# Optimization experiments

Measured on AMD Instinct MI355X. Metric: run time of the kernel, lower is better.

## Reference

```python
import jax, jax.numpy as jnp
import numpy as np

N_NODES = 100000
N_EDGES = 1600000
D = 64
BN_EPS = 1e-5


def setup_inputs() -> dict:
    key = jax.random.key(0)
    ks = jax.random.split(key, 10)
    s = 1.0 / np.sqrt(D)
    return {
        "features": jax.random.normal(ks[0], (N_NODES, D), dtype=jnp.float32),
        "src": jax.random.randint(ks[1], (N_EDGES,), 0, N_NODES, dtype=jnp.int32),
        "dst": jax.random.randint(ks[2], (N_EDGES,), 0, N_NODES, dtype=jnp.int32),
        "eps": jnp.zeros((), dtype=jnp.float32),
        "W1": jax.random.uniform(ks[3], (D, D), jnp.float32, -s, s),
        "b1": jax.random.uniform(ks[4], (D,), jnp.float32, -s, s),
        "W2": jax.random.uniform(ks[5], (D, D), jnp.float32, -s, s),
        "b2": jax.random.uniform(ks[6], (D,), jnp.float32, -s, s),
        "gamma": jnp.ones((D,), dtype=jnp.float32),
        "beta": jnp.zeros((D,), dtype=jnp.float32),
    }


def reference(features, src, dst, eps, W1, b1, W2, b2, gamma, beta):
    h_in = features
    # message passing: gather src node features, scatter-sum to dst (fn.copy_u + fn.sum)
    neigh = jax.ops.segment_sum(features[src], dst, num_segments=N_NODES)  # [N, D]
    # eps-weighted self term
    h = (1.0 + eps) * features + neigh
    # apply_func MLP: Linear -> ReLU -> Linear
    h = jnp.maximum(h @ W1 + b1, 0.0) @ W2 + b2
    # BatchNorm1d over nodes (training-mode batch statistics)
    mean = jnp.mean(h, axis=0)
    var = jnp.var(h, axis=0)
    h = (h - mean) * jax.lax.rsqrt(var + BN_EPS) * gamma + beta
    # activation
    h = jnp.maximum(h, 0.0)
    # residual (indim == outdim)
    h = h_in + h
    # dropout p=0 -> identity
    return h
```

## Files before the change

### kernel.cpp

```cpp
#include <hip/hip_runtime.h>
#include <hip/hip_fp16.h>

#define N_NODES 100000
#define N_EDGES 1600000
#define D 64
#define BN_EPS 1e-5f
#define NBKT 256
#define NPB 391
#define BKT_CAP 7680
#define SORT_T 1024
#define NSHARD 64

typedef _Float16 half8 __attribute__((ext_vector_type(8)));
typedef float f32x4 __attribute__((ext_vector_type(4)));

__global__ __launch_bounds__(256) void bucket_k(
    const int* __restrict__ src, const int* __restrict__ dst,
    int* __restrict__ bkt_cnt, int2* __restrict__ bktbuf)
{
    __shared__ int h[NBKT], base[NBKT], cur[NBKT];
    const int t = threadIdx.x;
    if (t < NBKT) { h[t] = 0; cur[t] = 0; }
    __syncthreads();
    const int e0 = blockIdx.x * 4096;
    int s[16], d[16], b[16];
    #pragma unroll
    for (int i = 0; i < 16; ++i) {
        int e = e0 + i * 256 + t;
        if (e < N_EDGES) {
            s[i] = src[e];
            d[i] = dst[e];
            b[i] = d[i] / NPB;
            atomicAdd(&h[b[i]], 1);
        } else {
            b[i] = -1;
        }
    }
    __syncthreads();
    if (t < NBKT) base[t] = atomicAdd(&bkt_cnt[t], h[t]);
    __syncthreads();
    #pragma unroll
    for (int i = 0; i < 16; ++i) {
        if (b[i] >= 0) {
            int p = atomicAdd(&cur[b[i]], 1);
            bktbuf[(size_t)b[i] * BKT_CAP + base[b[i]] + p] = make_int2(s[i], d[i]);
        }
    }
}

__global__ __launch_bounds__(SORT_T) void sort_k(
    const int2* __restrict__ bktbuf, const int* __restrict__ bkt_cnt,
    int* __restrict__ rowptr, int* __restrict__ col)
{
    __shared__ int h[NPB];
    __shared__ int cur[NPB];
    __shared__ int part[SORT_T];
    __shared__ int bsc[NBKT];

    const int b = blockIdx.x;
    const int t = threadIdx.x;
    const int nb0 = b * NPB;
    const int nodes_in = min(NPB, N_NODES - nb0);
    const int cnt = bkt_cnt[b];
    const int2* buf = bktbuf + (size_t)b * BKT_CAP;

    if (t < NBKT) bsc[t] = bkt_cnt[t];
    __syncthreads();
    for (int off = 1; off < NBKT; off <<= 1) {
        int x = 0;
        if (t < NBKT) {
            x = bsc[t];
            if (t >= off) x += bsc[t - off];
        }
        __syncthreads();
        if (t < NBKT) bsc[t] = x;
        __syncthreads();
    }
    const int gbase = bsc[b] - cnt;

    if (t < NPB) h[t] = 0;
    __syncthreads();

    for (int i = t; i < cnt; i += SORT_T)
        atomicAdd(&h[buf[i].y - nb0], 1);
    __syncthreads();

    int a = (t < NPB) ? h[t] : 0;
    part[t] = a;
    __syncthreads();
    for (int off = 1; off < SORT_T; off <<= 1) {
        int x = part[t];
        int u = (t >= off) ? part[t - off] : 0;
        __syncthreads();
        part[t] = x + u;
        __syncthreads();
    }
    int excl = part[t] - a;
    if (t < NPB) {
        cur[t] = excl;
        if (t < nodes_in) rowptr[nb0 + t] = gbase + excl;
    }
    if (b == NBKT - 1 && t == 0) rowptr[N_NODES] = N_EDGES;
    __syncthreads();

    for (int i = t; i < cnt; i += SORT_T) {
        int2 r = buf[i];
        int slot = atomicAdd(&cur[r.y - nb0], 1);
        col[gbase + slot] = r.x;
    }
}

__global__ __launch_bounds__(256) void conv_k(
    const float* __restrict__ feat, __half* __restrict__ feat16)
{
    size_t i = ((size_t)blockIdx.x * 256 + threadIdx.x) * 8;
    if (i < (size_t)N_NODES * D) {
        float4 v0 = *(const float4*)(feat + i);
        float4 v1 = *(const float4*)(feat + i + 4);
        __half2 o[4];
        o[0] = __floats2half2_rn(v0.x, v0.y);
        o[1] = __floats2half2_rn(v0.z, v0.w);
        o[2] = __floats2half2_rn(v1.x, v1.y);
        o[3] = __floats2half2_rn(v1.z, v1.w);
        *(float4*)(feat16 + i) = *(float4*)o;
    }
}

__global__ __launch_bounds__(256) void wprep_k(
    const float* __restrict__ W1, const float* __restrict__ W2,
    _Float16* __restrict__ w1t, _Float16* __restrict__ w2t)
{
    const int t = threadIdx.x;
    const int n = t >> 2;
    const int k0 = (t & 3) * 16;
    _Float16 o1[16], o2[16];
    #pragma unroll
    for (int j = 0; j < 16; ++j) {
        o1[j] = (_Float16)W1[(k0 + j) * 64 + n];
        o2[j] = (_Float16)W2[(k0 + j) * 64 + n];
    }
    #pragma unroll
    for (int j = 0; j < 16; j += 8) {
        *(half8*)(w1t + n * 64 + k0 + j) = *(half8*)&o1[j];
        *(half8*)(w2t + n * 64 + k0 + j) = *(half8*)&o2[j];
    }
}

__global__ __launch_bounds__(256) void gather16_k(
    const __half* __restrict__ feat16, const int* __restrict__ rowptr,
    const int* __restrict__ col, const float* __restrict__ epsp,
    __half* __restrict__ x16)
{
    int node = blockIdx.x * 4 + (threadIdx.x >> 6);
    int lane = threadIdx.x & 63;
    if (node >= N_NODES) return;
    int g = lane >> 3;
    int c = (lane & 7) << 3;
    int lo = rowptr[node];
    int hi = rowptr[node + 1];
    float a[8] = {0.f, 0.f, 0.f, 0.f, 0.f, 0.f, 0.f, 0.f};
    int e = lo + g;
    for (; e + 8 < hi; e += 16) {
        int s0 = col[e];
        int s1 = col[e + 8];
        float4 r0 = *(const float4*)(feat16 + (size_t)s0 * D + c);
        float4 r1 = *(const float4*)(feat16 + (size_t)s1 * D + c);
        const __half2* h0 = (const __half2*)&r0;
        const __half2* h1 = (const __half2*)&r1;
        #pragma unroll
        for (int i = 0; i < 4; ++i) {
            float2 f0 = __half22float2(h0[i]);
            float2 f1 = __half22float2(h1[i]);
            a[2 * i]     += f0.x + f1.x;
            a[2 * i + 1] += f0.y + f1.y;
        }
    }
    if (e < hi) {
        float4 r0 = *(const float4*)(feat16 + (size_t)col[e] * D + c);
        const __half2* h0 = (const __half2*)&r0;
        #pragma unroll
        for (int i = 0; i < 4; ++i) {
            float2 f0 = __half22float2(h0[i]);
            a[2 * i]     += f0.x;
            a[2 * i + 1] += f0.y;
        }
    }
    #pragma unroll
    for (int off = 8; off <= 32; off <<= 1)
        #pragma unroll
        for (int i = 0; i < 8; ++i)
            a[i] += __shfl_xor(a[i], off, 64);
    if (g == 0) {
        float4 rs = *(const float4*)(feat16 + (size_t)node * D + c);
        const __half2* hs = (const __half2*)&rs;
        const float epsv = 1.0f + epsp[0];
        __half2 o[4];
        #pragma unroll
        for (int i = 0; i < 4; ++i) {
            float2 fs = __half22float2(hs[i]);
            o[i] = __floats2half2_rn(fmaf(epsv, fs.x, a[2 * i]),
                                     fmaf(epsv, fs.y, a[2 * i + 1]));
        }
        *(float4*)(x16 + (size_t)node * D + c) = *(float4*)o;
    }
}

__global__ __launch_bounds__(256) void gather32_k(
    const float* __restrict__ feat, const int* __restrict__ rowptr,
    const int* __restrict__ col, const float* __restrict__ epsp,
    float* __restrict__ x)
{
    int node = blockIdx.x * 4 + (threadIdx.x >> 6);
    int lane = threadIdx.x & 63;
    if (node >= N_NODES) return;
    int g = lane >> 4;
    int c = (lane & 15) << 2;
    int lo = rowptr[node];
    int hi = rowptr[node + 1];
    float ax = 0.f, ay = 0.f, az = 0.f, aw = 0.f;
    int e = lo + g;
    for (; e + 4 < hi; e += 8) {
        int s0 = col[e];
        int s1 = col[e + 4];
        float4 v0 = *(const float4*)(feat + (size_t)s0 * D + c);
        float4 v1 = *(const float4*)(feat + (size_t)s1 * D + c);
        ax += v0.x; ay += v0.y; az += v0.z; aw += v0.w;
        ax += v1.x; ay += v1.y; az += v1.z; aw += v1.w;
    }
    if (e < hi) {
        float4 v = *(const float4*)(feat + (size_t)col[e] * D + c);
        ax += v.x; ay += v.y; az += v.z; aw += v.w;
    }
    #pragma unroll
    for (int off = 16; off <= 32; off <<= 1) {
        ax += __shfl_xor(ax, off, 64);
        ay += __shfl_xor(ay, off, 64);
        az += __shfl_xor(az, off, 64);
        aw += __shfl_xor(aw, off, 64);
    }
    if (g == 0) {
        float4 f = *(const float4*)(feat + (size_t)node * D + c);
        const float epsv = 1.0f + epsp[0];
        float4 r;
        r.x = fmaf(epsv, f.x, ax);
        r.y = fmaf(epsv, f.y, ay);
        r.z = fmaf(epsv, f.z, az);
        r.w = fmaf(epsv, f.w, aw);
        *(float4*)(x + (size_t)node * D + c) = r;
    }
}

__global__ __launch_bounds__(256) void mfma_mlp2_k(
    const __half* __restrict__ x16,
    const _Float16* __restrict__ w1t, const _Float16* __restrict__ w2t,
    const float* __restrict__ b1, const float* __restrict__ b2,
    __half* __restrict__ h216, float* __restrict__ stats)
{
    __shared__ __align__(16) _Float16 xts[64 * 72];

    const int t    = threadIdx.x;
    const int w    = t >> 6;
    const int lane = t & 63;
    const int m    = lane & 15;
    const int q    = lane >> 4;
    const int rbase = w * 16;
    const int nb   = blockIdx.x * 64;

    const _Float16* xg = (const _Float16*)x16 + (size_t)(nb + rbase + m) * 64 + q * 8;
    half8 a0 = *(const half8*)(xg);
    half8 a1 = *(const half8*)(xg + 32);

    f32x4 acc[4];
    #pragma unroll
    for (int jt = 0; jt < 4; ++jt) {
        const float bias = b1[jt * 16 + m];
        acc[jt] = (f32x4){bias, bias, bias, bias};
        const _Float16* bw = w1t + (jt * 16 + m) * 64 + q * 8;
        half8 bf0 = *(const half8*)(bw);
        half8 bf1 = *(const half8*)(bw + 32);
        acc[jt] = __builtin_amdgcn_mfma_f32_16x16x32_f16(a0, bf0, acc[jt], 0, 0, 0);
        acc[jt] = __builtin_amdgcn_mfma_f32_16x16x32_f16(a1, bf1, acc[jt], 0, 0, 0);
    }

    #pragma unroll
    for (int jt = 0; jt < 4; ++jt)
        #pragma unroll
        for (int r = 0; r < 4; ++r)
            xts[(rbase + q * 4 + r) * 72 + jt * 16 + m] =
                (_Float16)fmaxf(acc[jt][r], 0.0f);
    asm volatile("s_waitcnt lgkmcnt(0)" ::: "memory");

    const _Float16* xw = &xts[(rbase + m) * 72 + q * 8];
    half8 c0 = *(const half8*)(xw);
    half8 c1 = *(const half8*)(xw + 32);

    f32x4 acc2[4];
    #pragma unroll
    for (int jt = 0; jt < 4; ++jt) {
        const float bias = b2[jt * 16 + m];
        acc2[jt] = (f32x4){bias, bias, bias, bias};
        const _Float16* bw = w2t + (jt * 16 + m) * 64 + q * 8;
        half8 bf0 = *(const half8*)(bw);
        half8 bf1 = *(const half8*)(bw + 32);
        acc2[jt] = __builtin_amdgcn_mfma_f32_16x16x32_f16(c0, bf0, acc2[jt], 0, 0, 0);
        acc2[jt] = __builtin_amdgcn_mfma_f32_16x16x32_f16(c1, bf1, acc2[jt], 0, 0, 0);
    }
    asm volatile("s_waitcnt lgkmcnt(0)" ::: "memory");

    float psums[4], psqs[4];
    #pragma unroll
    for (int jt = 0; jt < 4; ++jt) {
        float ps = 0.f, pq = 0.f;
        #pragma unroll
        for (int r = 0; r < 4; ++r) {
            const int row = rbase + q * 4 + r;
            const float v = acc2[jt][r];
            const float vv = (nb + row < N_NODES) ? v : 0.f;
            ps += vv;
            pq += vv * vv;
            xts[row * 72 + jt * 16 + m] = (_Float16)v;
        }
        ps += __shfl_xor(ps, 16, 64); ps += __shfl_xor(ps, 32, 64);
        pq += __shfl_xor(pq, 16, 64); pq += __shfl_xor(pq, 32, 64);
        psums[jt] = ps; psqs[jt] = pq;
    }
    if (lane < 16) {
        float* sp = stats + (size_t)(blockIdx.x & (NSHARD - 1)) * 128;
        #pragma unroll
        for (int jt = 0; jt < 4; ++jt) {
            unsafeAtomicAdd(sp + jt * 16 + lane,      psums[jt]);
            unsafeAtomicAdd(sp + 64 + jt * 16 + lane, psqs[jt]);
        }
    }
    asm volatile("s_waitcnt lgkmcnt(0)" ::: "memory");

    {
        const int rr = lane >> 2;
        const int cc = (lane & 3) * 16;
        const int gn = nb + rbase + rr;
        if (gn < N_NODES) {
            float4 r0 = *(const float4*)&xts[(rbase + rr) * 72 + cc];
            float4 r1 = *(const float4*)&xts[(rbase + rr) * 72 + cc + 8];
            *(float4*)(h216 + (size_t)gn * 64 + cc)     = r0;
            *(float4*)(h216 + (size_t)gn * 64 + cc + 8) = r1;
        }
    }
}

__global__ __launch_bounds__(256) void mlp32_k(
    const float* __restrict__ x,
    const float* __restrict__ W1, const float* __restrict__ b1,
    const float* __restrict__ W2, const float* __restrict__ b2,
    float* __restrict__ h2out, float* __restrict__ stats)
{
    __shared__ float W1s[64 * 68];
    __shared__ float W2s[64 * 68];
    __shared__ float xs[64 * 65];
    __shared__ float b1s[64], b2s[64];

    const int t  = threadIdx.x;
    const int nb = blockIdx.x * 64;

    #pragma unroll
    for (int i = 0; i < 4; ++i) {
        int l  = t + i * 256;
        int k  = l >> 4;
        int j4 = (l & 15) << 2;
        *(float4*)(&W1s[k * 68 + j4]) = *(const float4*)(W1 + k * 64 + j4);
        *(float4*)(&W2s[k * 68 + j4]) = *(const float4*)(W2 + k * 64 + j4);
    }
    if (t < 64)       b1s[t]      = b1[t];
    else if (t < 128) b2s[t - 64] = b2[t - 64];

    #pragma unroll
    for (int i = 0; i < 2; ++i) {
        int n  = (t >> 3) + i * 32;
        int k8 = (t & 7) << 3;
        int gn = nb + n;
        float4 a = make_float4(0.f, 0.f, 0.f, 0.f), b = a;
        if (gn < N_NODES) {
            a = *(const float4*)(x + (size_t)gn * D + k8);
            b = *(const float4*)(x + (size_t)gn * D + k8 + 4);
        }
        *(float4*)&xs[n * 65 + k8]     = a;
        *(float4*)&xs[n * 65 + k8 + 4] = b;
    }
    __syncthreads();

    const int n0 = (t & 15) << 2;
    const int j0 = (t >> 4) << 2;
    const float* xr0 = &xs[(n0 + 0) * 65];
    const float* xr1 = &xs[(n0 + 1) * 65];
    const float* xr2 = &xs[(n0 + 2) * 65];
    const float* xr3 = &xs[(n0 + 3) * 65];

    float acc[4][4];
    #pragma unroll
    for (int a = 0; a < 4; ++a)
        #pragma unroll
        for (int b = 0; b < 4; ++b)
            acc[a][b] = b1s[j0 + b];

    #pragma unroll 8
    for (int k = 0; k < 64; ++k) {
        const float4 w = *(const float4*)(&W1s[k * 68 + j0]);
        const float x0 = xr0[k], x1 = xr1[k], x2 = xr2[k], x3 = xr3[k];
        acc[0][0] = fmaf(x0, w.x, acc[0][0]); acc[0][1] = fmaf(x0, w.y, acc[0][1]);
        acc[0][2] = fmaf(x0, w.z, acc[0][2]); acc[0][3] = fmaf(x0, w.w, acc[0][3]);
        acc[1][0] = fmaf(x1, w.x, acc[1][0]); acc[1][1] = fmaf(x1, w.y, acc[1][1]);
        acc[1][2] = fmaf(x1, w.z, acc[1][2]); acc[1][3] = fmaf(x1, w.w, acc[1][3]);
        acc[2][0] = fmaf(x2, w.x, acc[2][0]); acc[2][1] = fmaf(x2, w.y, acc[2][1]);
        acc[2][2] = fmaf(x2, w.z, acc[2][2]); acc[2][3] = fmaf(x2, w.w, acc[2][3]);
        acc[3][0] = fmaf(x3, w.x, acc[3][0]); acc[3][1] = fmaf(x3, w.y, acc[3][1]);
        acc[3][2] = fmaf(x3, w.z, acc[3][2]); acc[3][3] = fmaf(x3, w.w, acc[3][3]);
    }

    __syncthreads();
    #pragma unroll
    for (int a = 0; a < 4; ++a)
        #pragma unroll
        for (int b = 0; b < 4; ++b)
            xs[(n0 + a) * 65 + j0 + b] = fmaxf(acc[a][b], 0.0f);
    __syncthreads();

    float acc2[4][4];
    #pragma unroll
    for (int a = 0; a < 4; ++a)
        #pragma unroll
        for (int b = 0; b < 4; ++b)
            acc2[a][b] = b2s[j0 + b];

    #pragma unroll 8
    for (int k = 0; k < 64; ++k) {
        const float4 w = *(const float4*)(&W2s[k * 68 + j0]);
        const float x0 = xr0[k], x1 = xr1[k], x2 = xr2[k], x3 = xr3[k];
        acc2[0][0] = fmaf(x0, w.x, acc2[0][0]); acc2[0][1] = fmaf(x0, w.y, acc2[0][1]);
        acc2[0][2] = fmaf(x0, w.z, acc2[0][2]); acc2[0][3] = fmaf(x0, w.w, acc2[0][3]);
        acc2[1][0] = fmaf(x1, w.x, acc2[1][0]); acc2[1][1] = fmaf(x1, w.y, acc2[1][1]);
        acc2[1][2] = fmaf(x1, w.z, acc2[1][2]); acc2[1][3] = fmaf(x1, w.w, acc2[1][3]);
        acc2[2][0] = fmaf(x2, w.x, acc2[2][0]); acc2[2][1] = fmaf(x2, w.y, acc2[2][1]);
        acc2[2][2] = fmaf(x2, w.z, acc2[2][2]); acc2[2][3] = fmaf(x2, w.w, acc2[2][3]);
        acc2[3][0] = fmaf(x3, w.x, acc2[3][0]); acc2[3][1] = fmaf(x3, w.y, acc2[3][1]);
        acc2[3][2] = fmaf(x3, w.z, acc2[3][2]); acc2[3][3] = fmaf(x3, w.w, acc2[3][3]);
    }

    float psum[4] = {0.f, 0.f, 0.f, 0.f};
    float psq[4]  = {0.f, 0.f, 0.f, 0.f};
    #pragma unroll
    for (int a = 0; a < 4; ++a) {
        int gn = nb + n0 + a;
        if (gn < N_NODES) {
            float4 hh;
            hh.x = acc2[a][0]; hh.y = acc2[a][1]; hh.z = acc2[a][2]; hh.w = acc2[a][3];
            *(float4*)(h2out + (size_t)gn * 64 + j0) = hh;
            psum[0] += hh.x; psq[0] += hh.x * hh.x;
            psum[1] += hh.y; psq[1] += hh.y * hh.y;
            psum[2] += hh.z; psq[2] += hh.z * hh.z;
            psum[3] += hh.w; psq[3] += hh.w * hh.w;
        }
    }
    #pragma unroll
    for (int off = 8; off >= 1; off >>= 1)
        #pragma unroll
        for (int b = 0; b < 4; ++b) {
            psum[b] += __shfl_down(psum[b], off, 16);
            psq[b]  += __shfl_down(psq[b],  off, 16);
        }
    if ((t & 15) == 0) {
        float* sp = stats + (size_t)(blockIdx.x & (NSHARD - 1)) * 128;
        #pragma unroll
        for (int b = 0; b < 4; ++b) {
            unsafeAtomicAdd(sp + j0 + b,      psum[b]);
            unsafeAtomicAdd(sp + 64 + j0 + b, psq[b]);
        }
    }
}

__global__ void bnstats_k(const float* __restrict__ stats,
                          const float* __restrict__ gamma,
                          const float* __restrict__ beta,
                          float* __restrict__ sf)
{
    int j = threadIdx.x;
    float s = 0.f, q = 0.f;
    for (int c = 0; c < NSHARD; ++c) {
        s += stats[c * 128 + j];
        q += stats[c * 128 + 64 + j];
    }
    const float invN = 1.0f / (float)N_NODES;
    float mean  = s * invN;
    float var   = q * invN - mean * mean;
    float scale = gamma[j] * rsqrtf(var + BN_EPS);
    sf[j]      = scale;
    sf[64 + j] = beta[j] - mean * scale;
}

__global__ __launch_bounds__(256) void finish16_k(
    const float* __restrict__ feat, const __half* __restrict__ h216,
    const float* __restrict__ sf, float* __restrict__ out)
{
    __shared__ float scs[64], shs[64];
    if (threadIdx.x < 64) {
        scs[threadIdx.x] = sf[threadIdx.x];
        shs[threadIdx.x] = sf[64 + threadIdx.x];
    }
    __syncthreads();
    size_t i = (size_t)blockIdx.x * 256 + threadIdx.x;
    if (i < (size_t)N_NODES * D / 4) {
        int j = (int)((i * 4) & 63);
        const __half2* hp = (const __half2*)(h216 + i * 4);
        float2 h0 = __half22float2(hp[0]);
        float2 h1 = __half22float2(hp[1]);
        float4 f = *(const float4*)(feat + i * 4);
        float4 o;
        o.x = fmaxf(fmaf(h0.x, scs[j + 0], shs[j + 0]), 0.f) + f.x;
        o.y = fmaxf(fmaf(h0.y, scs[j + 1], shs[j + 1]), 0.f) + f.y;
        o.z = fmaxf(fmaf(h1.x, scs[j + 2], shs[j + 2]), 0.f) + f.z;
        o.w = fmaxf(fmaf(h1.y, scs[j + 3], shs[j + 3]), 0.f) + f.w;
        *(float4*)(out + i * 4) = o;
    }
}

__global__ __launch_bounds__(256) void finish_k(
    const float* __restrict__ feat, const float* __restrict__ sf,
    float* __restrict__ out)
{
    __shared__ float scs[64], shs[64];
    if (threadIdx.x < 64) {
        scs[threadIdx.x] = sf[threadIdx.x];
        shs[threadIdx.x] = sf[64 + threadIdx.x];
    }
    __syncthreads();
    size_t i = (size_t)blockIdx.x * 256 + threadIdx.x;
    if (i < (size_t)N_NODES * D / 4) {
        int j = (int)((i * 4) & 63);
        float4 h = *(float4*)(out + i * 4);
        float4 f = *(const float4*)(feat + i * 4);
        h.x = fmaxf(fmaf(h.x, scs[j + 0], shs[j + 0]), 0.f) + f.x;
        h.y = fmaxf(fmaf(h.y, scs[j + 1], shs[j + 1]), 0.f) + f.y;
        h.z = fmaxf(fmaf(h.z, scs[j + 2], shs[j + 2]), 0.f) + f.z;
        h.w = fmaxf(fmaf(h.w, scs[j + 3], shs[j + 3]), 0.f) + f.w;
        *(float4*)(out + i * 4) = h;
    }
}

extern "C" void kernel_launch(void* const* d_in, const int* in_sizes, int n_in,
                              void* d_out, int out_size, void* d_ws, size_t ws_size,
                              hipStream_t stream)
{
    const float* feat  = (const float*)d_in[0];
    const int*   src   = (const int*)d_in[1];
    const int*   dst   = (const int*)d_in[2];
    const float* eps   = (const float*)d_in[3];
    const float* W1    = (const float*)d_in[4];
    const float* b1    = (const float*)d_in[5];
    const float* W2    = (const float*)d_in[6];
    const float* b2    = (const float*)d_in[7];
    const float* gamma = (const float*)d_in[8];
    const float* beta  = (const float*)d_in[9];
    float* out = (float*)d_out;

    const size_t BKTSZ = (size_t)NBKT * BKT_CAP * sizeof(int2);
    const size_t F16SZ = (size_t)N_NODES * D * sizeof(__half);
    const size_t X32SZ = (size_t)N_NODES * D * sizeof(float);
    const size_t COLSZ = (size_t)N_EDGES * sizeof(int);
    const size_t RPSZ  = (size_t)(N_NODES + 1) * sizeof(int);
    const size_t STATSZ = (size_t)NSHARD * 128 * sizeof(float);
    const size_t TAIL  = STATSZ + NBKT * 4 + 128 * 4 + 2 * 4096 * sizeof(_Float16) + 256;
    const size_t need16 = BKTSZ + F16SZ + COLSZ + RPSZ + TAIL;

    if (ws_size >= need16) {
        char* p = (char*)d_ws;
        __half* x16    = (__half*)p;
        int2*   bktbuf = (int2*)p;
        __half* feat16 = (__half*)(p + BKTSZ);
        __half* h216   = (__half*)(p + BKTSZ);
        int*    col    = (int*)(p + BKTSZ + F16SZ);
        int*    rowptr = col + N_EDGES;
        float*  stats  = (float*)(rowptr + N_NODES + 1);
        int*    bkt_cnt = (int*)(stats + NSHARD * 128);
        float*  sf     = (float*)(bkt_cnt + NBKT);
        _Float16* w1t  = (_Float16*)(sf + 128);
        _Float16* w2t  = w1t + 4096;

        hipMemsetAsync(stats, 0, STATSZ + NBKT * 4, stream);
        conv_k<<<3125, 256, 0, stream>>>(feat, feat16);
        wprep_k<<<1, 256, 0, stream>>>(W1, W2, w1t, w2t);
        bucket_k<<<(N_EDGES + 4095) / 4096, 256, 0, stream>>>(src, dst, bkt_cnt, bktbuf);
        sort_k<<<NBKT, SORT_T, 0, stream>>>(bktbuf, bkt_cnt, rowptr, col);
        gather16_k<<<(N_NODES + 3) / 4, 256, 0, stream>>>(feat16, rowptr, col, eps, x16);
        mfma_mlp2_k<<<(N_NODES + 63) / 64, 256, 0, stream>>>(x16, w1t, w2t, b1, b2, h216, stats);
        bnstats_k<<<1, 64, 0, stream>>>(stats, gamma, beta, sf);
        finish16_k<<<(N_NODES * D / 4 + 255) / 256, 256, 0, stream>>>(feat, h216, sf, out);
    } else {
        char* p = (char*)d_ws;
        float* x32    = (float*)p;
        int2*  bktbuf = (int2*)p;
        int*   col    = (int*)(p + X32SZ);
        int*   rowptr = col + N_EDGES;
        float* stats  = (float*)(rowptr + N_NODES + 1);
        int*   bkt_cnt = (int*)(stats + NSHARD * 128);
        float* sf     = (float*)(bkt_cnt + NBKT);

        hipMemsetAsync(stats, 0, STATSZ + NBKT * 4, stream);
        bucket_k<<<(N_EDGES + 4095) / 4096, 256, 0, stream>>>(src, dst, bkt_cnt, bktbuf);
        sort_k<<<NBKT, SORT_T, 0, stream>>>(bktbuf, bkt_cnt, rowptr, col);
        gather32_k<<<(N_NODES + 3) / 4, 256, 0, stream>>>(feat, rowptr, col, eps, x32);
        mlp32_k<<<(N_NODES + 63) / 64, 256, 0, stream>>>(x32, W1, b1, W2, b2, out, stats);
        bnstats_k<<<1, 64, 0, stream>>>(stats, gamma, beta, sf);
        finish_k<<<(N_NODES * D / 4 + 255) / 256, 256, 0, stream>>>(feat, sf, out);
    }
}
```

Measured before the change: 221.9 us.

## Replace CSR sort+gather with bucketed LDS atomic scatter and fused prep kernel

Drops the full counting sort into CSR. Edges are now packed into 782 fine-grained buckets of 128 destination nodes each, storing src<<7|local_dst in a single int, inside a fused prep kernel that also does the fp16 feature conversion and the weight transpose. A new scatter kernel accumulates neighbour features into a swizzled LDS tile with shared-memory float atomics, then adds the eps self term and writes x16. This removes the sort pass, the rowptr/col arrays and two launches. In exchange it relies on LDS atomics and a fixed bucket capacity of 2560 that silently truncates if a bucket overflows.

```diff
diff --git a/kernel.cpp b/kernel.cpp
--- a/kernel.cpp
+++ b/kernel.cpp
@@ -5,22 +5,316 @@
 #define N_EDGES 1600000
 #define D 64
 #define BN_EPS 1e-5f
-#define NBKT 256
-#define NPB 391
-#define BKT_CAP 7680
+#define NSHARD 64
+
+#define NBKT 782
+#define NPB 128
+#define BKT_CAP 2560
+#define NBBLK 391
+#define ACC_LD 68
+
+#define ONBKT 256
+#define ONPB 391
+#define OCAP 7680
 #define SORT_T 1024
-#define NSHARD 64
 
 typedef _Float16 half8 __attribute__((ext_vector_type(8)));
 typedef float f32x4 __attribute__((ext_vector_type(4)));
 
-__global__ __launch_bounds__(256) void bucket_k(
+__global__ __launch_bounds__(256) void prep_k(
+    const int* __restrict__ src, const int* __restrict__ dst,
+    int* __restrict__ bkt_cnt, int* __restrict__ bktbuf,
+    const float* __restrict__ feat, __half* __restrict__ feat16,
+    const float* __restrict__ W1, const float* __restrict__ W2,
+    _Float16* __restrict__ w1t, _Float16* __restrict__ w2t)
+{
+    __shared__ int h[NBKT], base[NBKT], cur[NBKT];
+    const int blk = blockIdx.x;
+    const int t = threadIdx.x;
+
+    if (blk < NBBLK) {
+        for (int i = t; i < NBKT; i += 256) { h[i] = 0; cur[i] = 0; }
+        __syncthreads();
+        const int e0 = blk * 4096;
+        int pk[16], b[16];
+        #pragma unroll
+        for (int i = 0; i < 16; ++i) {
+            int e = e0 + i * 256 + t;
+            if (e < N_EDGES) {
+                int d = dst[e];
+                b[i] = d >> 7;
+                pk[i] = (src[e] << 7) | (d & 127);
+                atomicAdd(&h[b[i]], 1);
+            } else {
+                b[i] = -1;
+            }
+        }
+        __syncthreads();
+        for (int i = t; i < NBKT; i += 256)
+            if (h[i]) base[i] = atomicAdd(&bkt_cnt[i], h[i]);
+        __syncthreads();
+        #pragma unroll
+        for (int i = 0; i < 16; ++i) {
+            if (b[i] >= 0) {
+                int p = atomicAdd(&cur[b[i]], 1);
+                bktbuf[(size_t)b[i] * BKT_CAP + base[b[i]] + p] = pk[i];
+            }
+        }
+    } else if (blk < NBBLK + 3125) {
+        size_t i = ((size_t)(blk - NBBLK) * 256 + t) * 8;
+        if (i < (size_t)N_NODES * D) {
+            float4 v0 = *(const float4*)(feat + i);
+            float4 v1 = *(const float4*)(feat + i + 4);
+            __half2 o[4];
+            o[0] = __floats2half2_rn(v0.x, v0.y);
+            o[1] = __floats2half2_rn(v0.z, v0.w);
+            o[2] = __floats2half2_rn(v1.x, v1.y);
+            o[3] = __floats2half2_rn(v1.z, v1.w);
+            *(float4*)(feat16 + i) = *(float4*)o;
+        }
+    } else {
+        const int n = t >> 2;
+        const int k0 = (t & 3) * 16;
+        _Float16 o1[16], o2[16];
+        #pragma unroll
+        for (int j = 0; j < 16; ++j) {
+            o1[j] = (_Float16)W1[(k0 + j) * 64 + n];
+            o2[j] = (_Float16)W2[(k0 + j) * 64 + n];
+        }
+        #pragma unroll
+        for (int j = 0; j < 16; j += 8) {
+            *(half8*)(w1t + n * 64 + k0 + j) = *(half8*)&o1[j];
+            *(half8*)(w2t + n * 64 + k0 + j) = *(half8*)&o2[j];
+        }
+    }
+}
+
+__global__ __launch_bounds__(512, 8) void scatter16_k(
+    const int* __restrict__ bktbuf, const int* __restrict__ bkt_cnt,
+    const __half* __restrict__ feat16, const float* __restrict__ epsp,
+    __half* __restrict__ x16)
+{
+    __shared__ float acc[NPB * ACC_LD];
+    const int b = blockIdx.x;
+    const int t = threadIdx.x;
+    const int nb0 = b * NPB;
+    const int cnt = min(bkt_cnt[b], BKT_CAP);
+    const int* __restrict__ buf = bktbuf + (size_t)b * BKT_CAP;
+
+    for (int i = t; i < NPB * ACC_LD; i += 512) acc[i] = 0.f;
+    __syncthreads();
+
+    const int g0 = t >> 3;
+    const int k  = t & 7;
+    const int c  = k << 3;
+
+    int e = g0;
+    int pk = (e < cnt) ? buf[e] : 0;
+    while (e < cnt) {
+        const int en = e + 64;
+        const int pkn = (en < cnt) ? buf[en] : 0;
+        const int srow = pk >> 7;
+        const int drow = pk & 127;
+        float4 r = *(const float4*)(feat16 + (size_t)srow * 64 + c);
+        const __half2* hh = (const __half2*)&r;
+        float f[8];
+        #pragma unroll
+        for (int i = 0; i < 4; ++i) {
+            float2 fv = __half22float2(hh[i]);
+            f[2 * i]     = fv.x;
+            f[2 * i + 1] = fv.y;
+        }
+        float* rowp = acc + drow * ACC_LD + c;
+        const int xr = drow & 7;
+        #pragma unroll
+        for (int j = 0; j < 8; ++j)
+            atomicAdd(&rowp[j ^ xr], f[j]);
+        pk = pkn;
+        e = en;
+    }
+    __syncthreads();
+
+    const float epsv = 1.0f + epsp[0];
+    const int rr = t >> 2;
+    const int cc = (t & 3) << 4;
+    const int gn = nb0 + rr;
+    if (gn < N_NODES) {
+        const int xr = rr & 7;
+        const float* arow = acc + rr * ACC_LD;
+        const size_t gb = (size_t)gn * 64 + cc;
+        float4 s0 = *(const float4*)(feat16 + gb);
+        float4 s1 = *(const float4*)(feat16 + gb + 8);
+        const __half2* h0 = (const __half2*)&s0;
+        const __half2* h1 = (const __half2*)&s1;
+        __half2 o[8];
+        #pragma unroll
+        for (int i = 0; i < 4; ++i) {
+            float2 fs = __half22float2(h0[i]);
+            float a0 = arow[(cc + 2 * i)     ^ xr];
+            float a1 = arow[(cc + 2 * i + 1) ^ xr];
+            o[i] = __floats2half2_rn(fmaf(epsv, fs.x, a0), fmaf(epsv, fs.y, a1));
+        }
+        #pragma unroll
+        for (int i = 0; i < 4; ++i) {
+            float2 fs = __half22float2(h1[i]);
+            float a0 = arow[(cc + 8 + 2 * i)     ^ xr];
+            float a1 = arow[(cc + 8 + 2 * i + 1) ^ xr];
+            o[4 + i] = __floats2half2_rn(fmaf(epsv, fs.x, a0), fmaf(epsv, fs.y, a1));
+        }
+        *(float4*)(x16 + gb)     = *(float4*)&o[0];
+        *(float4*)(x16 + gb + 8) = *(float4*)&o[4];
+    }
+}
+
+__global__ __launch_bounds__(256) void mfma_mlp2_k(
+    const __half* __restrict__ x16,
+    const _Float16* __restrict__ w1t, const _Float16* __restrict__ w2t,
+    const float* __restrict__ b1, const float* __restrict__ b2,
+    __half* __restrict__ h216, float* __restrict__ stats)
+{
+    __shared__ __align__(16) _Float16 xts[64 * 72];
+
+    const int t    = threadIdx.x;
+    const int w    = t >> 6;
+    const int lane = t & 63;
+    const int m    = lane & 15;
+    const int q    = lane >> 4;
+    const int rbase = w * 16;
+    const int nb   = blockIdx.x * 64;
+
+    const _Float16* xg = (const _Float16*)x16 + (size_t)(nb + rbase + m) * 64 + q * 8;
+    half8 a0 = *(const half8*)(xg);
+    half8 a1 = *(const half8*)(xg + 32);
+
+    f32x4 acc[4];
+    #pragma unroll
+    for (int jt = 0; jt < 4; ++jt) {
+        const float bias = b1[jt * 16 + m];
+        acc[jt] = (f32x4){bias, bias, bias, bias};
+        const _Float16* bw = w1t + (jt * 16 + m) * 64 + q * 8;
+        half8 bf0 = *(const half8*)(bw);
+        half8 bf1 = *(const half8*)(bw + 32);
+        acc[jt] = __builtin_amdgcn_mfma_f32_16x16x32_f16(a0, bf0, acc[jt], 0, 0, 0);
+        acc[jt] = __builtin_amdgcn_mfma_f32_16x16x32_f16(a1, bf1, acc[jt], 0, 0, 0);
+    }
+
+    #pragma unroll
+    for (int jt = 0; jt < 4; ++jt)
+        #pragma unroll
+        for (int r = 0; r < 4; ++r)
+            xts[(rbase + q * 4 + r) * 72 + jt * 16 + m] =
+                (_Float16)fmaxf(acc[jt][r], 0.0f);
+    asm volatile("s_waitcnt lgkmcnt(0)" ::: "memory");
+
+    const _Float16* xw = &xts[(rbase + m) * 72 + q * 8];
+    half8 c0 = *(const half8*)(xw);
+    half8 c1 = *(const half8*)(xw + 32);
+
+    f32x4 acc2[4];
+    #pragma unroll
+    for (int jt = 0; jt < 4; ++jt) {
+        const float bias = b2[jt * 16 + m];
+        acc2[jt] = (f32x4){bias, bias, bias, bias};
+        const _Float16* bw = w2t + (jt * 16 + m) * 64 + q * 8;
+        half8 bf0 = *(const half8*)(bw);
+        half8 bf1 = *(const half8*)(bw + 32);
+        acc2[jt] = __builtin_amdgcn_mfma_f32_16x16x32_f16(c0, bf0, acc2[jt], 0, 0, 0);
+        acc2[jt] = __builtin_amdgcn_mfma_f32_16x16x32_f16(c1, bf1, acc2[jt], 0, 0, 0);
+    }
+    asm volatile("s_waitcnt lgkmcnt(0)" ::: "memory");
+
+    float psums[4], psqs[4];
+    #pragma unroll
+    for (int jt = 0; jt < 4; ++jt) {
+        float ps = 0.f, pq = 0.f;
+        #pragma unroll
+        for (int r = 0; r < 4; ++r) {
+            const int row = rbase + q * 4 + r;
+            const float v = acc2[jt][r];
+            const float vv = (nb + row < N_NODES) ? v : 0.f;
+            ps += vv;
+            pq += vv * vv;
+            xts[row * 72 + jt * 16 + m] = (_Float16)v;
+        }
+        ps += __shfl_xor(ps, 16, 64); ps += __shfl_xor(ps, 32, 64);
+        pq += __shfl_xor(pq, 16, 64); pq += __shfl_xor(pq, 32, 64);
+        psums[jt] = ps; psqs[jt] = pq;
+    }
+    if (lane < 16) {
+        float* sp = stats + (size_t)(blockIdx.x & (NSHARD - 1)) * 128;
+        #pragma unroll
+        for (int jt = 0; jt < 4; ++jt) {
+            unsafeAtomicAdd(sp + jt * 16 + lane,      psums[jt]);
+            unsafeAtomicAdd(sp + 64 + jt * 16 + lane, psqs[jt]);
+        }
+    }
+    asm volatile("s_waitcnt lgkmcnt(0)" ::: "memory");
+
+    {
+        const int rr = lane >> 2;
+        const int cc = (lane & 3) * 16;
+        const int gn = nb + rbase + rr;
+        if (gn < N_NODES) {
+            float4 r0 = *(const float4*)&xts[(rbase + rr) * 72 + cc];
+            float4 r1 = *(const float4*)&xts[(rbase + rr) * 72 + cc + 8];
+            *(float4*)(h216 + (size_t)gn * 64 + cc)     = r0;
+            *(float4*)(h216 + (size_t)gn * 64 + cc + 8) = r1;
+        }
+    }
+}
+
+__global__ void bnstats_k(const float* __restrict__ stats,
+                          const float* __restrict__ gamma,
+                          const float* __restrict__ beta,
+                          float* __restrict__ sf)
+{
+    int j = threadIdx.x;
+    float s = 0.f, q = 0.f;
+    for (int c = 0; c < NSHARD; ++c) {
+        s += stats[c * 128 + j];
+        q += stats[c * 128 + 64 + j];
+    }
+    const float invN = 1.0f / (float)N_NODES;
+    float mean  = s * invN;
+    float var   = q * invN - mean * mean;
+    float scale = gamma[j] * rsqrtf(var + BN_EPS);
+    sf[j]      = scale;
+    sf[64 + j] = beta[j] - mean * scale;
+}
+
+__global__ __launch_bounds__(256) void finish16_k(
+    const float* __restrict__ feat, const __half* __restrict__ h216,
+    const float* __restrict__ sf, float* __restrict__ out)
+{
+    __shared__ float scs[64], shs[64];
+    if (threadIdx.x < 64) {
+        scs[threadIdx.x] = sf[threadIdx.x];
+        shs[threadIdx.x] = sf[64 + threadIdx.x];
+    }
+    __syncthreads();
+    size_t i = (size_t)blockIdx.x * 256 + threadIdx.x;
+    if (i < (size_t)N_NODES * D / 4) {
+        int j = (int)((i * 4) & 63);
+        const __half2* hp = (const __half2*)(h216 + i * 4);
+        float2 h0 = __half22float2(hp[0]);
+        float2 h1 = __half22float2(hp[1]);
+        float4 f = *(const float4*)(feat + i * 4);
+        float4 o;
+        o.x = fmaxf(fmaf(h0.x, scs[j + 0], shs[j + 0]), 0.f) + f.x;
+        o.y = fmaxf(fmaf(h0.y, scs[j + 1], shs[j + 1]), 0.f) + f.y;
+        o.z = fmaxf(fmaf(h1.x, scs[j + 2], shs[j + 2]), 0.f) + f.z;
+        o.w = fmaxf(fmaf(h1.y, scs[j + 3], shs[j + 3]), 0.f) + f.w;
+        *(float4*)(out + i * 4) = o;
+    }
+}
+
+__global__ __launch_bounds__(256) void bucket2_k(
     const int* __restrict__ src, const int* __restrict__ dst,
     int* __restrict__ bkt_cnt, int2* __restrict__ bktbuf)
 {
-    __shared__ int h[NBKT], base[NBKT], cur[NBKT];
+    __shared__ int h[ONBKT], base[ONBKT], cur[ONBKT];
     const int t = threadIdx.x;
-    if (t < NBKT) { h[t] = 0; cur[t] = 0; }
+    if (t < ONBKT) { h[t] = 0; cur[t] = 0; }
     __syncthreads();
     const int e0 = blockIdx.x * 4096;
     int s[16], d[16], b[16];
@@ -30,20 +324,20 @@
         if (e < N_EDGES) {
             s[i] = src[e];
             d[i] = dst[e];
-            b[i] = d[i] / NPB;
+            b[i] = d[i] / ONPB;
             atomicAdd(&h[b[i]], 1);
         } else {
             b[i] = -1;
         }
     }
     __syncthreads();
-    if (t < NBKT) base[t] = atomicAdd(&bkt_cnt[t], h[t]);
+    if (t < ONBKT) base[t] = atomicAdd(&bkt_cnt[t], h[t]);
     __syncthreads();
     #pragma unroll
     for (int i = 0; i < 16; ++i) {
         if (b[i] >= 0) {
             int p = atomicAdd(&cur[b[i]], 1);
-            bktbuf[(size_t)b[i] * BKT_CAP + base[b[i]] + p] = make_int2(s[i], d[i]);
+            bktbuf[(size_t)b[i] * OCAP + base[b[i]] + p] = make_int2(s[i], d[i]);
         }
     }
 }
@@ -52,40 +346,40 @@
     const int2* __restrict__ bktbuf, const int* __restrict__ bkt_cnt,
     int* __restrict__ rowptr, int* __restrict__ col)
 {
-    __shared__ int h[NPB];
-    __shared__ int cur[NPB];
+    __shared__ int h[ONPB];
+    __shared__ int cur[ONPB];
     __shared__ int part[SORT_T];
-    __shared__ int bsc[NBKT];
+    __shared__ int bsc[ONBKT];
 
     const int b = blockIdx.x;
     const int t = threadIdx.x;
-    const int nb0 = b * NPB;
-    const int nodes_in = min(NPB, N_NODES - nb0);
+    const int nb0 = b * ONPB;
+    const int nodes_in = min(ONPB, N_NODES - nb0);
     const int cnt = bkt_cnt[b];
-    const int2* buf = bktbuf + (size_t)b * BKT_CAP;
-
-    if (t < NBKT) bsc[t] = bkt_cnt[t];
-    __syncthreads();
-    for (int off = 1; off < NBKT; off <<= 1) {
+    const int2* buf = bktbuf + (size_t)b * OCAP;
+
+    if (t < ONBKT) bsc[t] = bkt_cnt[t];
+    __syncthreads();
+    for (int off = 1; off < ONBKT; off <<= 1) {
         int x = 0;
-        if (t < NBKT) {
+        if (t < ONBKT) {
             x = bsc[t];
             if (t >= off) x += bsc[t - off];
         }
         __syncthreads();
-        if (t < NBKT) bsc[t] = x;
+        if (t < ONBKT) bsc[t] = x;
         __syncthreads();
     }
     const int gbase = bsc[b] - cnt;
 
-    if (t < NPB) h[t] = 0;
+    if (t < ONPB) h[t] = 0;
     __syncthreads();
 
     for (int i = t; i < cnt; i += SORT_T)
         atomicAdd(&h[buf[i].y - nb0], 1);
     __syncthreads();
 
-    int a = (t < NPB) ? h[t] : 0;
+    int a = (t < ONPB) ? h[t] : 0;
     part[t] = a;
     __syncthreads();
     for (int off = 1; off < SORT_T; off <<= 1) {
@@ -96,112 +390,17 @@
         __syncthreads();
     }
     int excl = part[t] - a;
-    if (t < NPB) {
+    if (t < ONPB) {
         cur[t] = excl;
         if (t < nodes_in) rowptr[nb0 + t] = gbase + excl;
     }
-    if (b == NBKT - 1 && t == 0) rowptr[N_NODES] = N_EDGES;
+    if (b == ONBKT - 1 && t == 0) rowptr[N_NODES] = N_EDGES;
     __syncthreads();
 
     for (int i = t; i < cnt; i += SORT_T) {
         int2 r = buf[i];
         int slot = atomicAdd(&cur[r.y - nb0], 1);
         col[gbase + slot] = r.x;
-    }
-}
-
-__global__ __launch_bounds__(256) void conv_k(
-    const float* __restrict__ feat, __half* __restrict__ feat16)
-{
-    size_t i = ((size_t)blockIdx.x * 256 + threadIdx.x) * 8;
-    if (i < (size_t)N_NODES * D) {
-        float4 v0 = *(const float4*)(feat + i);
-        float4 v1 = *(const float4*)(feat + i + 4);
-        __half2 o[4];
-        o[0] = __floats2half2_rn(v0.x, v0.y);
-        o[1] = __floats2half2_rn(v0.z, v0.w);
-        o[2] = __floats2half2_rn(v1.x, v1.y);
-        o[3] = __floats2half2_rn(v1.z, v1.w);
-        *(float4*)(feat16 + i) = *(float4*)o;
-    }
-}
-
-__global__ __launch_bounds__(256) void wprep_k(
-    const float* __restrict__ W1, const float* __restrict__ W2,
-    _Float16* __restrict__ w1t, _Float16* __restrict__ w2t)
-{
-    const int t = threadIdx.x;
-    const int n = t >> 2;
-    const int k0 = (t & 3) * 16;
-    _Float16 o1[16], o2[16];
-    #pragma unroll
-    for (int j = 0; j < 16; ++j) {
-        o1[j] = (_Float16)W1[(k0 + j) * 64 + n];
-        o2[j] = (_Float16)W2[(k0 + j) * 64 + n];
-    }
-    #pragma unroll
-    for (int j = 0; j < 16; j += 8) {
-        *(half8*)(w1t + n * 64 + k0 + j) = *(half8*)&o1[j];
-        *(half8*)(w2t + n * 64 + k0 + j) = *(half8*)&o2[j];
-    }
-}
-
-__global__ __launch_bounds__(256) void gather16_k(
-    const __half* __restrict__ feat16, const int* __restrict__ rowptr,
-    const int* __restrict__ col, const float* __restrict__ epsp,
-    __half* __restrict__ x16)
-{
-    int node = blockIdx.x * 4 + (threadIdx.x >> 6);
-    int lane = threadIdx.x & 63;
-    if (node >= N_NODES) return;
-    int g = lane >> 3;
-    int c = (lane & 7) << 3;
-    int lo = rowptr[node];
-    int hi = rowptr[node + 1];
-    float a[8] = {0.f, 0.f, 0.f, 0.f, 0.f, 0.f, 0.f, 0.f};
-    int e = lo + g;
-    for (; e + 8 < hi; e += 16) {
-        int s0 = col[e];
-        int s1 = col[e + 8];
-        float4 r0 = *(const float4*)(feat16 + (size_t)s0 * D + c);
-        float4 r1 = *(const float4*)(feat16 + (size_t)s1 * D + c);
-        const __half2* h0 = (const __half2*)&r0;
-        const __half2* h1 = (const __half2*)&r1;
-        #pragma unroll
-        for (int i = 0; i < 4; ++i) {
-            float2 f0 = __half22float2(h0[i]);
-            float2 f1 = __half22float2(h1[i]);
-            a[2 * i]     += f0.x + f1.x;
-            a[2 * i + 1] += f0.y + f1.y;
-        }
-    }
-    if (e < hi) {
-        float4 r0 = *(const float4*)(feat16 + (size_t)col[e] * D + c);
-        const __half2* h0 = (const __half2*)&r0;
-        #pragma unroll
-        for (int i = 0; i < 4; ++i) {
-            float2 f0 = __half22float2(h0[i]);
-            a[2 * i]     += f0.x;
-            a[2 * i + 1] += f0.y;
-        }
-    }
-    #pragma unroll
-    for (int off = 8; off <= 32; off <<= 1)
-        #pragma unroll
-        for (int i = 0; i < 8; ++i)
-            a[i] += __shfl_xor(a[i], off, 64);
-    if (g == 0) {
-        float4 rs = *(const float4*)(feat16 + (size_t)node * D + c);
-        const __half2* hs = (const __half2*)&rs;
-        const float epsv = 1.0f + epsp[0];
-        __half2 o[4];
-        #pragma unroll
-        for (int i = 0; i < 4; ++i) {
-            float2 fs = __half22float2(hs[i]);
-            o[i] = __floats2half2_rn(fmaf(epsv, fs.x, a[2 * i]),
-                                     fmaf(epsv, fs.y, a[2 * i + 1]));
-        }
-        *(float4*)(x16 + (size_t)node * D + c) = *(float4*)o;
     }
 }
 
@@ -250,103 +449,6 @@
     }
 }
 
-__global__ __launch_bounds__(256) void mfma_mlp2_k(
-    const __half* __restrict__ x16,
-    const _Float16* __restrict__ w1t, const _Float16* __restrict__ w2t,
-    const float* __restrict__ b1, const float* __restrict__ b2,
-    __half* __restrict__ h216, float* __restrict__ stats)
-{
-    __shared__ __align__(16) _Float16 xts[64 * 72];
-
-    const int t    = threadIdx.x;
-    const int w    = t >> 6;
-    const int lane = t & 63;
-    const int m    = lane & 15;
-    const int q    = lane >> 4;
-    const int rbase = w * 16;
-    const int nb   = blockIdx.x * 64;
-
-    const _Float16* xg = (const _Float16*)x16 + (size_t)(nb + rbase + m) * 64 + q * 8;
-    half8 a0 = *(const half8*)(xg);
-    half8 a1 = *(const half8*)(xg + 32);
-
-    f32x4 acc[4];
-    #pragma unroll
-    for (int jt = 0; jt < 4; ++jt) {
-        const float bias = b1[jt * 16 + m];
-        acc[jt] = (f32x4){bias, bias, bias, bias};
-        const _Float16* bw = w1t + (jt * 16 + m) * 64 + q * 8;
-        half8 bf0 = *(const half8*)(bw);
-        half8 bf1 = *(const half8*)(bw + 32);
-        acc[jt] = __builtin_amdgcn_mfma_f32_16x16x32_f16(a0, bf0, acc[jt], 0, 0, 0);
-        acc[jt] = __builtin_amdgcn_mfma_f32_16x16x32_f16(a1, bf1, acc[jt], 0, 0, 0);
-    }
-
-    #pragma unroll
-    for (int jt = 0; jt < 4; ++jt)
-        #pragma unroll
-        for (int r = 0; r < 4; ++r)
-            xts[(rbase + q * 4 + r) * 72 + jt * 16 + m] =
-                (_Float16)fmaxf(acc[jt][r], 0.0f);
-    asm volatile("s_waitcnt lgkmcnt(0)" ::: "memory");
-
-    const _Float16* xw = &xts[(rbase + m) * 72 + q * 8];
-    half8 c0 = *(const half8*)(xw);
-    half8 c1 = *(const half8*)(xw + 32);
-
-    f32x4 acc2[4];
-    #pragma unroll
-    for (int jt = 0; jt < 4; ++jt) {
-        const float bias = b2[jt * 16 + m];
-        acc2[jt] = (f32x4){bias, bias, bias, bias};
-        const _Float16* bw = w2t + (jt * 16 + m) * 64 + q * 8;
-        half8 bf0 = *(const half8*)(bw);
-        half8 bf1 = *(const half8*)(bw + 32);
-        acc2[jt] = __builtin_amdgcn_mfma_f32_16x16x32_f16(c0, bf0, acc2[jt], 0, 0, 0);
-        acc2[jt] = __builtin_amdgcn_mfma_f32_16x16x32_f16(c1, bf1, acc2[jt], 0, 0, 0);
-    }
-    asm volatile("s_waitcnt lgkmcnt(0)" ::: "memory");
-
-    float psums[4], psqs[4];
-    #pragma unroll
-    for (int jt = 0; jt < 4; ++jt) {
-        float ps = 0.f, pq = 0.f;
-        #pragma unroll
-        for (int r = 0; r < 4; ++r) {
-            const int row = rbase + q * 4 + r;
-            const float v = acc2[jt][r];
-            const float vv = (nb + row < N_NODES) ? v : 0.f;
-            ps += vv;
-            pq += vv * vv;
-            xts[row * 72 + jt * 16 + m] = (_Float16)v;
-        }
-        ps += __shfl_xor(ps, 16, 64); ps += __shfl_xor(ps, 32, 64);
-        pq += __shfl_xor(pq, 16, 64); pq += __shfl_xor(pq, 32, 64);
-        psums[jt] = ps; psqs[jt] = pq;
-    }
-    if (lane < 16) {
-        float* sp = stats + (size_t)(blockIdx.x & (NSHARD - 1)) * 128;
-        #pragma unroll
-        for (int jt = 0; jt < 4; ++jt) {
-            unsafeAtomicAdd(sp + jt * 16 + lane,      psums[jt]);
-            unsafeAtomicAdd(sp + 64 + jt * 16 + lane, psqs[jt]);
-        }
-    }
-    asm volatile("s_waitcnt lgkmcnt(0)" ::: "memory");
-
-    {
-        const int rr = lane >> 2;
-        const int cc = (lane & 3) * 16;
-        const int gn = nb + rbase + rr;
-        if (gn < N_NODES) {
-            float4 r0 = *(const float4*)&xts[(rbase + rr) * 72 + cc];
-            float4 r1 = *(const float4*)&xts[(rbase + rr) * 72 + cc + 8];
-            *(float4*)(h216 + (size_t)gn * 64 + cc)     = r0;
-            *(float4*)(h216 + (size_t)gn * 64 + cc + 8) = r1;
-        }
-    }
-}
-
 __global__ __launch_bounds__(256) void mlp32_k(
     const float* __restrict__ x,
     const float* __restrict__ W1, const float* __restrict__ b1,
@@ -476,51 +578,6 @@
     }
 }
 
-__global__ void bnstats_k(const float* __restrict__ stats,
-                          const float* __restrict__ gamma,
-                          const float* __restrict__ beta,
-                          float* __restrict__ sf)
-{
-    int j = threadIdx.x;
-    float s = 0.f, q = 0.f;
-    for (int c = 0; c < NSHARD; ++c) {
-        s += stats[c * 128 + j];
-        q += stats[c * 128 + 64 + j];
-    }
-    const float invN = 1.0f / (float)N_NODES;
-    float mean  = s * invN;
-    float var   = q * invN - mean * mean;
-    float scale = gamma[j] * rsqrtf(var + BN_EPS);
-    sf[j]      = scale;
-    sf[64 + j] = beta[j] - mean * scale;
-}
-
-__global__ __launch_bounds__(256) void finish16_k(
-    const float* __restrict__ feat, const __half* __restrict__ h216,
-    const float* __restrict__ sf, float* __restrict__ out)
-{
-    __shared__ float scs[64], shs[64];
-    if (threadIdx.x < 64) {
-        scs[threadIdx.x] = sf[threadIdx.x];
-        shs[threadIdx.x] = sf[64 + threadIdx.x];
-    }
-    __syncthreads();
-    size_t i = (size_t)blockIdx.x * 256 + threadIdx.x;
-    if (i < (size_t)N_NODES * D / 4) {
-        int j = (int)((i * 4) & 63);
-        const __half2* hp = (const __half2*)(h216 + i * 4);
-        float2 h0 = __half22float2(hp[0]);
-        float2 h1 = __half22float2(hp[1]);
-        float4 f = *(const float4*)(feat + i * 4);
-        float4 o;
-        o.x = fmaxf(fmaf(h0.x, scs[j + 0], shs[j + 0]), 0.f) + f.x;
-        o.y = fmaxf(fmaf(h0.y, scs[j + 1], shs[j + 1]), 0.f) + f.y;
-        o.z = fmaxf(fmaf(h1.x, scs[j + 2], shs[j + 2]), 0.f) + f.z;
-        o.w = fmaxf(fmaf(h1.y, scs[j + 3], shs[j + 3]), 0.f) + f.w;
-        *(float4*)(out + i * 4) = o;
-    }
-}
-
 __global__ __launch_bounds__(256) void finish_k(
     const float* __restrict__ feat, const float* __restrict__ sf,
     float* __restrict__ out)
@@ -560,39 +617,35 @@
     const float* beta  = (const float*)d_in[9];
     float* out = (float*)d_out;
 
-    const size_t BKTSZ = (size_t)NBKT * BKT_CAP * sizeof(int2);
-    const size_t F16SZ = (size_t)N_NODES * D * sizeof(__half);
-    const size_t X32SZ = (size_t)N_NODES * D * sizeof(float);
-    const size_t COLSZ = (size_t)N_EDGES * sizeof(int);
-    const size_t RPSZ  = (size_t)(N_NODES + 1) * sizeof(int);
+    const size_t BKTSZ  = (size_t)NBKT * BKT_CAP * sizeof(int);
+    const size_t F16SZ  = (size_t)N_NODES * D * sizeof(__half);
+    const size_t X16SZ  = F16SZ + 8192;
     const size_t STATSZ = (size_t)NSHARD * 128 * sizeof(float);
-    const size_t TAIL  = STATSZ + NBKT * 4 + 128 * 4 + 2 * 4096 * sizeof(_Float16) + 256;
-    const size_t need16 = BKTSZ + F16SZ + COLSZ + RPSZ + TAIL;
-
-    if (ws_size >= need16) {
+    const size_t CNTSZ  = (size_t)((NBKT + 15) & ~15) * sizeof(int);
+    const size_t TAIL   = STATSZ + CNTSZ + 128 * 4 + 2 * 4096 * sizeof(_Float16) + 256;
+    const size_t need   = BKTSZ + F16SZ + X16SZ + TAIL;
+
+    if (ws_size >= need) {
         char* p = (char*)d_ws;
-        __half* x16    = (__half*)p;
-        int2*   bktbuf = (int2*)p;
-        __half* feat16 = (__half*)(p + BKTSZ);
-        __half* h216   = (__half*)(p + BKTSZ);
-        int*    col    = (int*)(p + BKTSZ + F16SZ);
-        int*    rowptr = col + N_EDGES;
-        float*  stats  = (float*)(rowptr + N_NODES + 1);
+        int*    bktbuf  = (int*)p;
+        __half* feat16  = (__half*)(p + BKTSZ);
+        __half* h216    = feat16;
+        __half* x16     = (__half*)(p + BKTSZ + F16SZ);
+        float*  stats   = (float*)(p + BKTSZ + F16SZ + X16SZ);
         int*    bkt_cnt = (int*)(stats + NSHARD * 128);
-        float*  sf     = (float*)(bkt_cnt + NBKT);
-        _Float16* w1t  = (_Float16*)(sf + 128);
-        _Float16* w2t  = w1t + 4096;
-
-        hipMemsetAsync(stats, 0, STATSZ + NBKT * 4, stream);
-        conv_k<<<3125, 256, 0, stream>>>(feat, feat16);
-        wprep_k<<<1, 256, 0, stream>>>(W1, W2, w1t, w2t);
-        bucket_k<<<(N_EDGES + 4095) / 4096, 256, 0, stream>>>(src, dst, bkt_cnt, bktbuf);
-        sort_k<<<NBKT, SORT_T, 0, stream>>>(bktbuf, bkt_cnt, rowptr, col);
-        gather16_k<<<(N_NODES + 3) / 4, 256, 0, stream>>>(feat16, rowptr, col, eps, x16);
+        float*  sf      = (float*)((char*)bkt_cnt + CNTSZ);
+        _Float16* w1t   = (_Float16*)(sf + 128);
+        _Float16* w2t   = w1t + 4096;
+
+        hipMemsetAsync(stats, 0, STATSZ + CNTSZ, stream);
+        prep_k<<<NBBLK + 3125 + 1, 256, 0, stream>>>(src, dst, bkt_cnt, bktbuf,
+                                                     feat, feat16, W1, W2, w1t, w2t);
+        scatter16_k<<<NBKT, 512, 0, stream>>>(bktbuf, bkt_cnt, feat16, eps, x16);
         mfma_mlp2_k<<<(N_NODES + 63) / 64, 256, 0, stream>>>(x16, w1t, w2t, b1, b2, h216, stats);
         bnstats_k<<<1, 64, 0, stream>>>(stats, gamma, beta, sf);
         finish16_k<<<(N_NODES * D / 4 + 255) / 256, 256, 0, stream>>>(feat, h216, sf, out);
     } else {
+        const size_t X32SZ = (size_t)N_NODES * D * sizeof(float);
         char* p = (char*)d_ws;
         float* x32    = (float*)p;
         int2*  bktbuf = (int2*)p;
@@ -600,11 +653,11 @@
         int*   rowptr = col + N_EDGES;
         float* stats  = (float*)(rowptr + N_NODES + 1);
         int*   bkt_cnt = (int*)(stats + NSHARD * 128);
-        float* sf     = (float*)(bkt_cnt + NBKT);
-
-        hipMemsetAsync(stats, 0, STATSZ + NBKT * 4, stream);
-        bucket_k<<<(N_EDGES + 4095) / 4096, 256, 0, stream>>>(src, dst, bkt_cnt, bktbuf);
-        sort_k<<<NBKT, SORT_T, 0, stream>>>(bktbuf, bkt_cnt, rowptr, col);
+        float* sf     = (float*)(bkt_cnt + ONBKT);
+
+        hipMemsetAsync(stats, 0, STATSZ + ONBKT * 4, stream);
+        bucket2_k<<<(N_EDGES + 4095) / 4096, 256, 0, stream>>>(src, dst, bkt_cnt, bktbuf);
+        sort_k<<<ONBKT, SORT_T, 0, stream>>>(bktbuf, bkt_cnt, rowptr, col);
         gather32_k<<<(N_NODES + 3) / 4, 256, 0, stream>>>(feat, rowptr, col, eps, x32);
         mlp32_k<<<(N_NODES + 63) / 64, 256, 0, stream>>>(x32, W1, b1, W2, b2, out, stats);
         bnstats_k<<<1, 64, 0, stream>>>(stats, gamma, beta, sf);
```

New measurement: 826.2 us. 3.72x slower.
